# Kernel optimization log

Measured on AMD Instinct MI355X. Metric: run time of the kernel, lower is better.

The kernel has to match this reference:

```python
import jax, jax.numpy as jnp
import numpy as np

NEG_SLOPE = 0.2  # PyG GATConv LeakyReLU slope
BN_EPS = 1e-5
NUM_GRAPHS = 16


def gat_conv(x, src, dst, W, a_src, a_dst, bias, heads, out_c, concat):
    N = x.shape[0]
    h = (x @ W).reshape(N, heads, out_c)                      # [N,H,C]
    s_src = jnp.sum(h * a_src, axis=-1)                       # [N,H] per-node src score
    s_dst = jnp.sum(h * a_dst, axis=-1)                       # [N,H]
    e = jax.nn.leaky_relu(s_src[src] + s_dst[dst], NEG_SLOPE) # [E,H]
    # segment softmax over incoming edges of each dst node
    m = jax.ops.segment_max(e, dst, num_segments=N)           # [N,H]
    ex = jnp.exp(e - m[dst])
    denom = jax.ops.segment_sum(ex, dst, num_segments=N)      # [N,H]
    alpha = ex / (denom[dst] + 1e-16)                         # [E,H]
    msg = h[src] * alpha[:, :, None]                          # [E,H,C]
    out = jax.ops.segment_sum(msg, dst, num_segments=N)       # [N,H,C]
    out = out.reshape(N, heads * out_c) if concat else out.mean(axis=1)
    return out + bias


def batchnorm_eval(x, gamma, beta, rm, rv):
    return (x - rm) * jax.lax.rsqrt(rv + BN_EPS) * gamma + beta


def setup_inputs() -> dict:
    key = jax.random.key(0)
    ks = jax.random.split(key, 16)
    N, E, Fin, Hc, Hd, Emb = 20000, 640000, 128, 64, 4, 128
    x = jax.random.normal(ks[0], (N, Fin), dtype=jnp.float32)
    edge_index = jax.random.randint(ks[1], (2, E), 0, N, dtype=jnp.int64)
    batch = jnp.sort(jax.random.randint(ks[2], (N,), 0, NUM_GRAPHS, dtype=jnp.int64))
    sc1 = 1.0 / np.sqrt(Fin)
    sc2 = 1.0 / np.sqrt(Hc * Hd)
    return {
        "x": x, "edge_index": edge_index, "batch": batch,
        "W1": jax.random.normal(ks[3], (Fin, Hd * Hc), dtype=jnp.float32) * sc1,
        "a_src1": jax.random.normal(ks[4], (Hd, Hc), dtype=jnp.float32) * sc2,
        "a_dst1": jax.random.normal(ks[5], (Hd, Hc), dtype=jnp.float32) * sc2,
        "b1": jnp.zeros((Hd * Hc,), jnp.float32),
        "g1": jnp.ones((Hd * Hc,), jnp.float32),
        "be1": jnp.zeros((Hd * Hc,), jnp.float32),
        "rm1": jax.random.normal(ks[6], (Hd * Hc,), dtype=jnp.float32) * 0.1,
        "rv1": jnp.ones((Hd * Hc,), jnp.float32),
        "W2": jax.random.normal(ks[7], (Hd * Hc, Emb), dtype=jnp.float32) * sc2,
        "a_src2": jax.random.normal(ks[8], (1, Emb), dtype=jnp.float32) / np.sqrt(Emb),
        "a_dst2": jax.random.normal(ks[9], (1, Emb), dtype=jnp.float32) / np.sqrt(Emb),
        "b2": jnp.zeros((Emb,), jnp.float32),
        "g2": jnp.ones((Emb,), jnp.float32),
        "be2": jnp.zeros((Emb,), jnp.float32),
        "rm2": jax.random.normal(ks[10], (Emb,), dtype=jnp.float32) * 0.1,
        "rv2": jnp.ones((Emb,), jnp.float32),
    }


def reference(x, edge_index, batch, W1, a_src1, a_dst1, b1, g1, be1, rm1, rv1,
              W2, a_src2, a_dst2, b2, g2, be2, rm2, rv2):
    N = x.shape[0]
    loops = jnp.arange(N, dtype=edge_index.dtype)
    src = jnp.concatenate([edge_index[0], loops])  # PyG GATConv adds self-loops
    dst = jnp.concatenate([edge_index[1], loops])
    # layer 1: heads=4, concat
    h = gat_conv(x, src, dst, W1, a_src1, a_dst1, b1, heads=4, out_c=64, concat=True)
    h = batchnorm_eval(h, g1, be1, rm1, rv1)
    h = jax.nn.elu(h)  # dropout is identity in eval mode
    # layer 2: heads=1, no concat (mean over heads)
    h = gat_conv(h, src, dst, W2, a_src2, a_dst2, b2, heads=1, out_c=128, concat=False)
    h = batchnorm_eval(h, g2, be2, rm2, rv2)
    # global mean pool per graph
    sums = jax.ops.segment_sum(h, batch, num_segments=NUM_GRAPHS)
    cnts = jax.ops.segment_sum(jnp.ones((N,), h.dtype), batch, num_segments=NUM_GRAPHS)
    return sums / jnp.maximum(cnts, 1.0)[:, None]
```

## Files before the change

kernel.cpp:

```cpp
#include <hip/hip_runtime.h>
#include <hip/hip_bf16.h>
#include <math.h>

#define NEG_SLOPE 0.2f
#define BN_EPS 1e-5f
#define ELLW 128
#define SCLAMP 60.0f
#define LDP 68

typedef __attribute__((ext_vector_type(8))) short bf16x8;
typedef __attribute__((ext_vector_type(4))) float f32x4;

__device__ __forceinline__ void atomAddF(float* p, float v) { unsafeAtomicAdd(p, v); }
__device__ __forceinline__ float bf_lo(unsigned u) { return __uint_as_float(u << 16); }
__device__ __forceinline__ float bf_hi(unsigned u) { return __uint_as_float(u & 0xffff0000u); }
__device__ __forceinline__ float lk(float x) { return x > 0.f ? x : NEG_SLOPE * x; }
__device__ __forceinline__ float eexp(float x) { return __expf(fminf(x, SCLAMP)); }
__device__ __forceinline__ unsigned packbf(float lo, float hi) {
    return (unsigned)__bfloat16_as_ushort(__float2bfloat16(lo)) |
           ((unsigned)__bfloat16_as_ushort(__float2bfloat16(hi)) << 16);
}

__global__ __launch_bounds__(256) void prep_kernel(const float* __restrict__ x,
                                                   const float* __restrict__ W1,
                                                   const float* __restrict__ W2,
                                                   __hip_bfloat16* __restrict__ xbf,
                                                   __hip_bfloat16* __restrict__ WT1,
                                                   __hip_bfloat16* __restrict__ WT2,
                                                   int* __restrict__ zb, int zwords,
                                                   int n4) {
    int i = blockIdx.x * blockDim.x + threadIdx.x;
    if (i < n4) {
        float4 v = ((const float4*)x)[i];
        ushort4 st;
        st.x = __bfloat16_as_ushort(__float2bfloat16(v.x));
        st.y = __bfloat16_as_ushort(__float2bfloat16(v.y));
        st.z = __bfloat16_as_ushort(__float2bfloat16(v.z));
        st.w = __bfloat16_as_ushort(__float2bfloat16(v.w));
        *(ushort4*)(xbf + (size_t)i * 4) = st;
        return;
    }
    int j = i - n4;
    if (j < 128 * 256) {
        int k = j >> 8, n = j & 255;
        WT1[(size_t)n * 128 + k] = __float2bfloat16(W1[j]);
        return;
    }
    j -= 128 * 256;
    if (j < 256 * 128) {
        int k = j >> 7, n = j & 127;
        WT2[(size_t)n * 256 + k] = __float2bfloat16(W2[j]);
        return;
    }
    j -= 256 * 128;
    if (j < zwords) zb[j] = 0;
}

__global__ __launch_bounds__(256) void scatter_kernel(const int* __restrict__ src,
                                                      const int* __restrict__ dst,
                                                      int* __restrict__ cnt,
                                                      unsigned short* __restrict__ ell,
                                                      int N, int E, int Etot) {
    const int xcd = blockIdx.x & 7;
    const int slice = blockIdx.x >> 3;
    const int nslices = gridDim.x >> 3;
    const int d0 = (int)((long)xcd * N / 8);
    const int d1 = (int)((long)(xcd + 1) * N / 8);
    for (int e = slice * 256 + threadIdx.x; e < Etot; e += nslices * 256) {
        int d = (e < E) ? dst[e] : e - E;
        if (d < d0 || d >= d1) continue;
        int s = (e < E) ? src[e] : d;
        int pos = atomicAdd(cnt + d, 1);
        if (pos < ELLW) ell[(size_t)d * ELLW + pos] = (unsigned short)s;
    }
}

__global__ __launch_bounds__(256) void gemm_score_kernel(const __hip_bfloat16* __restrict__ A,
                                                         const __hip_bfloat16* __restrict__ BT,
                                                         __hip_bfloat16* __restrict__ C,
                                                         const float* __restrict__ asrc,
                                                         const float* __restrict__ adst,
                                                         float* __restrict__ ssrc,
                                                         float* __restrict__ sdst,
                                                         int M, int N, int K, int heads) {
    __shared__ __hip_bfloat16 As[64 * LDP];
    __shared__ __hip_bfloat16 Bs[64 * LDP];
    const int tid = threadIdx.x;
    const int w = tid >> 6;
    const int lane = tid & 63;
    const int q = lane >> 4;
    const int r16 = lane & 15;
    const int bm = blockIdx.y * 64;
    const int bn = blockIdx.x * 64;
    const int lrow = tid >> 3;
    const int lseg = tid & 7;
    f32x4 acc[4] = {};

    for (int k0 = 0; k0 < K; k0 += 64) {
#pragma unroll
        for (int half = 0; half < 2; ++half) {
            int row = lrow + half * 32;
            int ga = min(bm + row, M - 1);
            *(bf16x8*)(&As[row * LDP + lseg * 8]) =
                *(const bf16x8*)(A + (size_t)ga * K + k0 + lseg * 8);
            *(bf16x8*)(&Bs[row * LDP + lseg * 8]) =
                *(const bf16x8*)(BT + (size_t)(bn + row) * K + k0 + lseg * 8);
        }
        __syncthreads();
#pragma unroll
        for (int kk = 0; kk < 64; kk += 32) {
            bf16x8 a = *(const bf16x8*)(&As[(w * 16 + r16) * LDP + kk + q * 8]);
#pragma unroll
            for (int t = 0; t < 4; ++t) {
                bf16x8 b = *(const bf16x8*)(&Bs[(t * 16 + r16) * LDP + kk + q * 8]);
                acc[t] = __builtin_amdgcn_mfma_f32_16x16x32_bf16(a, b, acc[t], 0, 0, 0);
            }
        }
        __syncthreads();
    }
#pragma unroll
    for (int t = 0; t < 4; ++t)
#pragma unroll
        for (int r = 0; r < 4; ++r) {
            int row = bm + w * 16 + q * 4 + r;
            if (row < M)
                C[(size_t)row * N + bn + t * 16 + r16] = __float2bfloat16(acc[t][r]);
        }
    if (heads) {
        const int h = (heads == 4) ? blockIdx.x : 0;
        float asv[4], adv[4];
#pragma unroll
        for (int t = 0; t < 4; ++t) {
            int col = bn + t * 16 + r16;
            asv[t] = asrc[col]; adv[t] = adst[col];
        }
#pragma unroll
        for (int r = 0; r < 4; ++r) {
            int row = bm + w * 16 + q * 4 + r;
            float ss = 0.f, sd = 0.f;
#pragma unroll
            for (int t = 0; t < 4; ++t) { ss += acc[t][r] * asv[t]; sd += acc[t][r] * adv[t]; }
#pragma unroll
            for (int mask = 1; mask <= 8; mask <<= 1) {
                ss += __shfl_xor(ss, mask);
                sd += __shfl_xor(sd, mask);
            }
            if (r16 == 0 && row < M) {
                atomAddF(&ssrc[(size_t)row * heads + h], ss);
                atomAddF(&sdst[(size_t)row * heads + h], sd);
            }
        }
    }
}

__global__ __launch_bounds__(256) void fused1_kernel(const unsigned short* __restrict__ ell,
                                                     const int* __restrict__ cnt,
                                                     const float* __restrict__ ssrc,
                                                     const float* __restrict__ sdst,
                                                     const __hip_bfloat16* __restrict__ h1,
                                                     const float* __restrict__ b,
                                                     const float* __restrict__ g,
                                                     const float* __restrict__ be,
                                                     const float* __restrict__ rm,
                                                     const float* __restrict__ rv,
                                                     __hip_bfloat16* __restrict__ out1,
                                                     int N) {
    __shared__ float sex[4][ELLW * 4];
    __shared__ unsigned soff[4][ELLW];
    const int w = threadIdx.x >> 6;
    const int lane = threadIdx.x & 63;
    const int n = blockIdx.x * 4 + w;
    if (n >= N) return;
    const int degn = min(cnt[n], ELLW);
    const unsigned short* __restrict__ row = ell + (size_t)n * ELLW;
    const float4 sd4 = *(const float4*)(sdst + (size_t)n * 4);

    float4 d4 = {0.f, 0.f, 0.f, 0.f};
    for (int i = lane; i < degn; i += 64) {
        int s = row[i];
        float4 sc = *(const float4*)(ssrc + (size_t)s * 4);
        float4 e4;
        e4.x = eexp(lk(sc.x + sd4.x)); e4.y = eexp(lk(sc.y + sd4.y));
        e4.z = eexp(lk(sc.z + sd4.z)); e4.w = eexp(lk(sc.w + sd4.w));
        *(float4*)(&sex[w][i * 4]) = e4;
        soff[w][i] = (unsigned)s << 9;
        d4.x += e4.x; d4.y += e4.y; d4.z += e4.z; d4.w += e4.w;
    }
    if (lane == 0 && (degn & 1)) {
        float4 z = {0.f, 0.f, 0.f, 0.f};
        *(float4*)(&sex[w][degn * 4]) = z;
        soff[w][degn] = 0;
    }
#pragma unroll
    for (int o = 32; o; o >>= 1) {
        d4.x += __shfl_xor(d4.x, o); d4.y += __shfl_xor(d4.y, o);
        d4.z += __shfl_xor(d4.z, o); d4.w += __shfl_xor(d4.w, o);
    }

    const int half = lane >> 5;
    const int l32 = lane & 31;
    const int ch = l32 * 8;
    const int h = l32 >> 3;
    const unsigned choff = (unsigned)(l32 * 16);
    const float denh = h == 0 ? d4.x : h == 1 ? d4.y : h == 2 ? d4.z : d4.w;
    const float rden = 1.f / (denh + 1e-16f);
    const unsigned char* __restrict__ hb = (const unsigned char*)h1;
    const int degp = (degn + 1) & ~1;

    f32x4 a0 = {0.f, 0.f, 0.f, 0.f}, a1 = {0.f, 0.f, 0.f, 0.f};
    int i = 0;
    for (; i + 8 <= degp; i += 8) {
        unsigned off[4]; float av[4]; uint4 u[4];
#pragma unroll
        for (int k = 0; k < 4; ++k) {
            int e = i + 2 * k + half;
            off[k] = soff[w][e] + choff;
            av[k] = sex[w][e * 4 + h];
        }
#pragma unroll
        for (int k = 0; k < 4; ++k) u[k] = *(const uint4*)(hb + off[k]);
#pragma unroll
        for (int k = 0; k < 4; ++k) {
            a0.x += av[k] * bf_lo(u[k].x); a0.y += av[k] * bf_hi(u[k].x);
            a0.z += av[k] * bf_lo(u[k].y); a0.w += av[k] * bf_hi(u[k].y);
            a1.x += av[k] * bf_lo(u[k].z); a1.y += av[k] * bf_hi(u[k].z);
            a1.z += av[k] * bf_lo(u[k].w); a1.w += av[k] * bf_hi(u[k].w);
        }
    }
    for (; i < degp; i += 2) {
        int e = i + half;
        unsigned off = soff[w][e] + choff;
        float av = sex[w][e * 4 + h];
        uint4 u = *(const uint4*)(hb + off);
        a0.x += av * bf_lo(u.x); a0.y += av * bf_hi(u.x);
        a0.z += av * bf_lo(u.y); a0.w += av * bf_hi(u.y);
        a1.x += av * bf_lo(u.z); a1.y += av * bf_hi(u.z);
        a1.z += av * bf_lo(u.w); a1.w += av * bf_hi(u.w);
    }
    a0.x += __shfl_xor(a0.x, 32); a0.y += __shfl_xor(a0.y, 32);
    a0.z += __shfl_xor(a0.z, 32); a0.w += __shfl_xor(a0.w, 32);
    a1.x += __shfl_xor(a1.x, 32); a1.y += __shfl_xor(a1.y, 32);
    a1.z += __shfl_xor(a1.z, 32); a1.w += __shfl_xor(a1.w, 32);

    float4 bb0 = *(const float4*)(b + ch),  bb1 = *(const float4*)(b + ch + 4);
    float4 gg0 = *(const float4*)(g + ch),  gg1 = *(const float4*)(g + ch + 4);
    float4 ee0 = *(const float4*)(be + ch), ee1 = *(const float4*)(be + ch + 4);
    float4 mm0 = *(const float4*)(rm + ch), mm1 = *(const float4*)(rm + ch + 4);
    float4 vv0 = *(const float4*)(rv + ch), vv1 = *(const float4*)(rv + ch + 4);
    float o0 = (a0.x * rden + bb0.x - mm0.x) * rsqrtf(vv0.x + BN_EPS) * gg0.x + ee0.x;
    float o1 = (a0.y * rden + bb0.y - mm0.y) * rsqrtf(vv0.y + BN_EPS) * gg0.y + ee0.y;
    float o2 = (a0.z * rden + bb0.z - mm0.z) * rsqrtf(vv0.z + BN_EPS) * gg0.z + ee0.z;
    float o3 = (a0.w * rden + bb0.w - mm0.w) * rsqrtf(vv0.w + BN_EPS) * gg0.w + ee0.w;
    float o4 = (a1.x * rden + bb1.x - mm1.x) * rsqrtf(vv1.x + BN_EPS) * gg1.x + ee1.x;
    float o5 = (a1.y * rden + bb1.y - mm1.y) * rsqrtf(vv1.y + BN_EPS) * gg1.y + ee1.y;
    float o6 = (a1.z * rden + bb1.z - mm1.z) * rsqrtf(vv1.z + BN_EPS) * gg1.z + ee1.z;
    float o7 = (a1.w * rden + bb1.w - mm1.w) * rsqrtf(vv1.w + BN_EPS) * gg1.w + ee1.w;
    o0 = o0 > 0.f ? o0 : expm1f(o0); o1 = o1 > 0.f ? o1 : expm1f(o1);
    o2 = o2 > 0.f ? o2 : expm1f(o2); o3 = o3 > 0.f ? o3 : expm1f(o3);
    o4 = o4 > 0.f ? o4 : expm1f(o4); o5 = o5 > 0.f ? o5 : expm1f(o5);
    o6 = o6 > 0.f ? o6 : expm1f(o6); o7 = o7 > 0.f ? o7 : expm1f(o7);
    if (half == 0) {
        uint4 st;
        st.x = packbf(o0, o1); st.y = packbf(o2, o3);
        st.z = packbf(o4, o5); st.w = packbf(o6, o7);
        *(uint4*)(out1 + (size_t)n * 256 + ch) = st;
    }
}

__global__ __launch_bounds__(256) void fused2_kernel(const unsigned short* __restrict__ ell,
                                                     const int* __restrict__ cnt,
                                                     const float* __restrict__ ssrc,
                                                     const float* __restrict__ sdst,
                                                     const __hip_bfloat16* __restrict__ h2,
                                                     const float* __restrict__ b,
                                                     const float* __restrict__ g,
                                                     const float* __restrict__ be,
                                                     const float* __restrict__ rm,
                                                     const float* __restrict__ rv,
                                                     __hip_bfloat16* __restrict__ out2,
                                                     int N) {
    __shared__ float sex[4][ELLW];
    __shared__ unsigned soff[4][ELLW];
    const int w = threadIdx.x >> 6;
    const int lane = threadIdx.x & 63;
    const int n = blockIdx.x * 4 + w;
    if (n >= N) return;
    const int degn = min(cnt[n], ELLW);
    const unsigned short* __restrict__ row = ell + (size_t)n * ELLW;
    const float sd = sdst[n];

    float den = 0.f;
    for (int i = lane; i < degn; i += 64) {
        int s = row[i];
        float e = eexp(lk(ssrc[s] + sd));
        sex[w][i] = e;
        soff[w][i] = (unsigned)s << 8;
        den += e;
    }
    if (lane == 0 && (degn & 1)) { sex[w][degn] = 0.f; soff[w][degn] = 0; }
#pragma unroll
    for (int o = 32; o; o >>= 1) den += __shfl_xor(den, o);
    const float rden = 1.f / (den + 1e-16f);

    const int half = lane >> 5;
    const int l32 = lane & 31;
    const int ch = l32 * 4;
    const unsigned choff = (unsigned)(l32 * 8);
    const unsigned char* __restrict__ hb = (const unsigned char*)h2;
    const int degp = (degn + 1) & ~1;

    f32x4 acc = {0.f, 0.f, 0.f, 0.f};
    int i = 0;
    for (; i + 8 <= degp; i += 8) {
        unsigned off[4]; float av[4]; uint2 u[4];
#pragma unroll
        for (int k = 0; k < 4; ++k) {
            int e = i + 2 * k + half;
            off[k] = soff[w][e] + choff;
            av[k] = sex[w][e];
        }
#pragma unroll
        for (int k = 0; k < 4; ++k) u[k] = *(const uint2*)(hb + off[k]);
#pragma unroll
        for (int k = 0; k < 4; ++k) {
            acc.x += av[k] * bf_lo(u[k].x); acc.y += av[k] * bf_hi(u[k].x);
            acc.z += av[k] * bf_lo(u[k].y); acc.w += av[k] * bf_hi(u[k].y);
        }
    }
    for (; i < degp; i += 2) {
        int e = i + half;
        unsigned off = soff[w][e] + choff;
        float av = sex[w][e];
        uint2 u = *(const uint2*)(hb + off);
        acc.x += av * bf_lo(u.x); acc.y += av * bf_hi(u.x);
        acc.z += av * bf_lo(u.y); acc.w += av * bf_hi(u.y);
    }
    acc.x += __shfl_xor(acc.x, 32); acc.y += __shfl_xor(acc.y, 32);
    acc.z += __shfl_xor(acc.z, 32); acc.w += __shfl_xor(acc.w, 32);

    if (half == 0) {
        float4 bb = *(const float4*)(b + ch), gg = *(const float4*)(g + ch);
        float4 ee = *(const float4*)(be + ch), mm = *(const float4*)(rm + ch);
        float4 vv = *(const float4*)(rv + ch);
        float o0 = (acc.x * rden + bb.x - mm.x) * rsqrtf(vv.x + BN_EPS) * gg.x + ee.x;
        float o1 = (acc.y * rden + bb.y - mm.y) * rsqrtf(vv.y + BN_EPS) * gg.y + ee.y;
        float o2 = (acc.z * rden + bb.z - mm.z) * rsqrtf(vv.z + BN_EPS) * gg.z + ee.z;
        float o3 = (acc.w * rden + bb.w - mm.w) * rsqrtf(vv.w + BN_EPS) * gg.w + ee.w;
        ushort2 s01, s23;
        s01.x = __bfloat16_as_ushort(__float2bfloat16(o0));
        s01.y = __bfloat16_as_ushort(__float2bfloat16(o1));
        s23.x = __bfloat16_as_ushort(__float2bfloat16(o2));
        s23.y = __bfloat16_as_ushort(__float2bfloat16(o3));
        uint2 st = { *(unsigned*)&s01, *(unsigned*)&s23 };
        *(uint2*)(out2 + (size_t)n * 128 + ch) = st;
    }
}

__global__ __launch_bounds__(128) void pool_kernel(const __hip_bfloat16* __restrict__ out2,
                                                   const int* __restrict__ batch,
                                                   float* __restrict__ pool,
                                                   int N, int npb) {
    const int j = threadIdx.x;
    int n0 = blockIdx.x * npb;
    int n1 = min(n0 + npb, N);
    if (n0 >= n1) return;
    int curg = batch[n0];
    float acc = 0.f;
    for (int n = n0; n < n1; ++n) {
        int gr = batch[n];
        if (gr != curg) {
            atomAddF(pool + (size_t)curg * 128 + j, acc);
            acc = 0.f; curg = gr;
        }
        acc += __bfloat162float(out2[(size_t)n * 128 + j]);
    }
    atomAddF(pool + (size_t)curg * 128 + j, acc);
}

__device__ __forceinline__ int lowerBound(const int* __restrict__ a, int n, int v) {
    int lo = 0, hi = n;
    while (lo < hi) {
        int mid = (lo + hi) >> 1;
        if (a[mid] < v) lo = mid + 1; else hi = mid;
    }
    return lo;
}

__global__ __launch_bounds__(256) void final_kernel(const float* __restrict__ pool,
                                                    const int* __restrict__ batch,
                                                    float* __restrict__ out, int N) {
    int i = blockIdx.x * blockDim.x + threadIdx.x;
    int g = i >> 7;
    int c = lowerBound(batch, N, g + 1) - lowerBound(batch, N, g);
    out[i] = pool[i] / fmaxf((float)c, 1.f);
}

extern "C" void kernel_launch(void* const* d_in, const int* in_sizes, int n_in,
                              void* d_out, int out_size, void* d_ws, size_t ws_size,
                              hipStream_t stream) {
    const float* x    = (const float*)d_in[0];
    const int* ei     = (const int*)d_in[1];
    const int* batch  = (const int*)d_in[2];
    const float* W1   = (const float*)d_in[3];
    const float* as1  = (const float*)d_in[4];
    const float* ad1  = (const float*)d_in[5];
    const float* b1   = (const float*)d_in[6];
    const float* g1   = (const float*)d_in[7];
    const float* be1  = (const float*)d_in[8];
    const float* rm1  = (const float*)d_in[9];
    const float* rv1  = (const float*)d_in[10];
    const float* W2   = (const float*)d_in[11];
    const float* as2  = (const float*)d_in[12];
    const float* ad2  = (const float*)d_in[13];
    const float* b2   = (const float*)d_in[14];
    const float* g2   = (const float*)d_in[15];
    const float* be2  = (const float*)d_in[16];
    const float* rm2  = (const float*)d_in[17];
    const float* rv2  = (const float*)d_in[18];
    float* out = (float*)d_out;

    const int N = in_sizes[0] / 128;
    const int E = in_sizes[1] / 2;
    const int Etot = E + N;
    const int* src = ei;
    const int* dst = ei + E;

    char* p = (char*)d_ws;
    auto alloc = [&](size_t bytes) { char* r = p; p += (bytes + 255) & ~(size_t)255; return r; };
    __hip_bfloat16* h1   = (__hip_bfloat16*)alloc((size_t)N * 256 * 2);
    __hip_bfloat16* out1 = (__hip_bfloat16*)alloc((size_t)N * 256 * 2);
    __hip_bfloat16* out2 = (__hip_bfloat16*)alloc((size_t)N * 128 * 2);
    __hip_bfloat16* xbf  = (__hip_bfloat16*)alloc((size_t)N * 128 * 2);
    __hip_bfloat16* WT1  = (__hip_bfloat16*)alloc(256 * 128 * 2);
    __hip_bfloat16* WT2  = (__hip_bfloat16*)alloc(128 * 256 * 2);
    const int zwords     = N * 10 + 2048 + N;
    char* zbase          = alloc((size_t)zwords * 4);
    float* ssrc1         = (float*)zbase;
    float* sdst1         = ssrc1 + (size_t)N * 4;
    float* ssrc2         = sdst1 + (size_t)N * 4;
    float* sdst2         = ssrc2 + N;
    float* pool          = sdst2 + N;
    int*   cnt           = (int*)(pool + 2048);
    unsigned short* ell  = (unsigned short*)alloc((size_t)N * ELLW * 2);
    __hip_bfloat16* h2   = h1;

    const int n4 = N * 128 / 4;
    const int ptot = n4 + 2 * 128 * 256 + zwords;
    prep_kernel<<<(ptot + 255) / 256, 256, 0, stream>>>(x, W1, W2, xbf, WT1, WT2,
                                                        (int*)zbase, zwords, n4);
    scatter_kernel<<<2048, 256, 0, stream>>>(src, dst, cnt, ell, N, E, Etot);

    gemm_score_kernel<<<dim3(256 / 64, (N + 63) / 64), 256, 0, stream>>>(
        xbf, WT1, h1, as1, ad1, ssrc1, sdst1, N, 256, 128, 4);
    fused1_kernel<<<(N + 3) / 4, 256, 0, stream>>>(ell, cnt, ssrc1, sdst1, h1,
                                                   b1, g1, be1, rm1, rv1, out1, N);
    gemm_score_kernel<<<dim3(128 / 64, (N + 63) / 64), 256, 0, stream>>>(
        out1, WT2, h2, as2, ad2, ssrc2, sdst2, N, 128, 256, 1);
    fused2_kernel<<<(N + 3) / 4, 256, 0, stream>>>(ell, cnt, ssrc2, sdst2, h2,
                                                   b2, g2, be2, rm2, rv2, out2, N);

    pool_kernel<<<(N + 19) / 20, 128, 0, stream>>>(out2, batch, pool, N, 20);
    final_kernel<<<8, 256, 0, stream>>>(pool, batch, out, N);
}
```

Baseline: 234.6 us.

## Merge edge scatter with layer-1 GEMM in one launch; deepen gather unroll

The edge-to-ELL scatter and the first GEMM+score kernel are independent, so they are merged into one launch. The first nbg blocks do GEMM tiles and the remaining 2048 do scatter, letting both run concurrently and saving one launch. The aggregation loops in both fused kernels now unroll 8 gathers per iteration instead of 4 to keep more memory loads in flight. In exchange, scatter blocks carry the GEMM's shared-memory footprint, and the deeper unroll raises register pressure. The XCD partitioning for scatter now comes from gb&7 rather than a dense block index, which still maps consistently.

```diff
diff --git a/kernel.cpp b/kernel.cpp
--- a/kernel.cpp
+++ b/kernel.cpp
@@ -56,14 +56,107 @@
     if (j < zwords) zb[j] = 0;
 }
 
-__global__ __launch_bounds__(256) void scatter_kernel(const int* __restrict__ src,
-                                                      const int* __restrict__ dst,
-                                                      int* __restrict__ cnt,
-                                                      unsigned short* __restrict__ ell,
-                                                      int N, int E, int Etot) {
-    const int xcd = blockIdx.x & 7;
-    const int slice = blockIdx.x >> 3;
-    const int nslices = gridDim.x >> 3;
+__device__ __forceinline__ void gemm_body(const __hip_bfloat16* __restrict__ A,
+                                          const __hip_bfloat16* __restrict__ BT,
+                                          __hip_bfloat16* __restrict__ C,
+                                          const float* __restrict__ asrc,
+                                          const float* __restrict__ adst,
+                                          float* __restrict__ ssrc,
+                                          float* __restrict__ sdst,
+                                          int M, int N, int K, int heads,
+                                          int bx, int by) {
+    __shared__ __hip_bfloat16 As[64 * LDP];
+    __shared__ __hip_bfloat16 Bs[64 * LDP];
+    const int tid = threadIdx.x;
+    const int w = tid >> 6;
+    const int lane = tid & 63;
+    const int q = lane >> 4;
+    const int r16 = lane & 15;
+    const int bm = by * 64;
+    const int bn = bx * 64;
+    const int lrow = tid >> 3;
+    const int lseg = tid & 7;
+    f32x4 acc[4] = {};
+
+    for (int k0 = 0; k0 < K; k0 += 64) {
+#pragma unroll
+        for (int half = 0; half < 2; ++half) {
+            int row = lrow + half * 32;
+            int ga = min(bm + row, M - 1);
+            *(bf16x8*)(&As[row * LDP + lseg * 8]) =
+                *(const bf16x8*)(A + (size_t)ga * K + k0 + lseg * 8);
+            *(bf16x8*)(&Bs[row * LDP + lseg * 8]) =
+                *(const bf16x8*)(BT + (size_t)(bn + row) * K + k0 + lseg * 8);
+        }
+        __syncthreads();
+#pragma unroll
+        for (int kk = 0; kk < 64; kk += 32) {
+            bf16x8 a = *(const bf16x8*)(&As[(w * 16 + r16) * LDP + kk + q * 8]);
+#pragma unroll
+            for (int t = 0; t < 4; ++t) {
+                bf16x8 b = *(const bf16x8*)(&Bs[(t * 16 + r16) * LDP + kk + q * 8]);
+                acc[t] = __builtin_amdgcn_mfma_f32_16x16x32_bf16(a, b, acc[t], 0, 0, 0);
+            }
+        }
+        __syncthreads();
+    }
+#pragma unroll
+    for (int t = 0; t < 4; ++t)
+#pragma unroll
+        for (int r = 0; r < 4; ++r) {
+            int row = bm + w * 16 + q * 4 + r;
+            if (row < M)
+                C[(size_t)row * N + bn + t * 16 + r16] = __float2bfloat16(acc[t][r]);
+        }
+    if (heads) {
+        const int h = (heads == 4) ? bx : 0;
+        float asv[4], adv[4];
+#pragma unroll
+        for (int t = 0; t < 4; ++t) {
+            int col = bn + t * 16 + r16;
+            asv[t] = asrc[col]; adv[t] = adst[col];
+        }
+#pragma unroll
+        for (int r = 0; r < 4; ++r) {
+            int row = bm + w * 16 + q * 4 + r;
+            float ss = 0.f, sd = 0.f;
+#pragma unroll
+            for (int t = 0; t < 4; ++t) { ss += acc[t][r] * asv[t]; sd += acc[t][r] * adv[t]; }
+#pragma unroll
+            for (int mask = 1; mask <= 8; mask <<= 1) {
+                ss += __shfl_xor(ss, mask);
+                sd += __shfl_xor(sd, mask);
+            }
+            if (r16 == 0 && row < M) {
+                atomAddF(&ssrc[(size_t)row * heads + h], ss);
+                atomAddF(&sdst[(size_t)row * heads + h], sd);
+            }
+        }
+    }
+}
+
+__global__ __launch_bounds__(256) void sg1_kernel(const __hip_bfloat16* __restrict__ A,
+                                                  const __hip_bfloat16* __restrict__ BT,
+                                                  __hip_bfloat16* __restrict__ C,
+                                                  const float* __restrict__ asrc,
+                                                  const float* __restrict__ adst,
+                                                  float* __restrict__ ssrc,
+                                                  float* __restrict__ sdst,
+                                                  int M, int nbg,
+                                                  const int* __restrict__ src,
+                                                  const int* __restrict__ dst,
+                                                  int* __restrict__ cnt,
+                                                  unsigned short* __restrict__ ell,
+                                                  int N, int E, int Etot) {
+    const int gb = blockIdx.x;
+    if (gb < nbg) {
+        gemm_body(A, BT, C, asrc, adst, ssrc, sdst, M, 256, 128, 4, gb & 3, gb >> 2);
+        return;
+    }
+    const int xcd = gb & 7;
+    const int sb = gb - nbg;
+    const int slice = sb >> 3;
+    const int nslices = (gridDim.x - nbg) >> 3;
     const int d0 = (int)((long)xcd * N / 8);
     const int d1 = (int)((long)(xcd + 1) * N / 8);
     for (int e = slice * 256 + threadIdx.x; e < Etot; e += nslices * 256) {
@@ -83,74 +176,7 @@
                                                          float* __restrict__ ssrc,
                                                          float* __restrict__ sdst,
                                                          int M, int N, int K, int heads) {
-    __shared__ __hip_bfloat16 As[64 * LDP];
-    __shared__ __hip_bfloat16 Bs[64 * LDP];
-    const int tid = threadIdx.x;
-    const int w = tid >> 6;
-    const int lane = tid & 63;
-    const int q = lane >> 4;
-    const int r16 = lane & 15;
-    const int bm = blockIdx.y * 64;
-    const int bn = blockIdx.x * 64;
-    const int lrow = tid >> 3;
-    const int lseg = tid & 7;
-    f32x4 acc[4] = {};
-
-    for (int k0 = 0; k0 < K; k0 += 64) {
-#pragma unroll
-        for (int half = 0; half < 2; ++half) {
-            int row = lrow + half * 32;
-            int ga = min(bm + row, M - 1);
-            *(bf16x8*)(&As[row * LDP + lseg * 8]) =
-                *(const bf16x8*)(A + (size_t)ga * K + k0 + lseg * 8);
-            *(bf16x8*)(&Bs[row * LDP + lseg * 8]) =
-                *(const bf16x8*)(BT + (size_t)(bn + row) * K + k0 + lseg * 8);
-        }
-        __syncthreads();
-#pragma unroll
-        for (int kk = 0; kk < 64; kk += 32) {
-            bf16x8 a = *(const bf16x8*)(&As[(w * 16 + r16) * LDP + kk + q * 8]);
-#pragma unroll
-            for (int t = 0; t < 4; ++t) {
-                bf16x8 b = *(const bf16x8*)(&Bs[(t * 16 + r16) * LDP + kk + q * 8]);
-                acc[t] = __builtin_amdgcn_mfma_f32_16x16x32_bf16(a, b, acc[t], 0, 0, 0);
-            }
-        }
-        __syncthreads();
-    }
-#pragma unroll
-    for (int t = 0; t < 4; ++t)
-#pragma unroll
-        for (int r = 0; r < 4; ++r) {
-            int row = bm + w * 16 + q * 4 + r;
-            if (row < M)
-                C[(size_t)row * N + bn + t * 16 + r16] = __float2bfloat16(acc[t][r]);
-        }
-    if (heads) {
-        const int h = (heads == 4) ? blockIdx.x : 0;
-        float asv[4], adv[4];
-#pragma unroll
-        for (int t = 0; t < 4; ++t) {
-            int col = bn + t * 16 + r16;
-            asv[t] = asrc[col]; adv[t] = adst[col];
-        }
-#pragma unroll
-        for (int r = 0; r < 4; ++r) {
-            int row = bm + w * 16 + q * 4 + r;
-            float ss = 0.f, sd = 0.f;
-#pragma unroll
-            for (int t = 0; t < 4; ++t) { ss += acc[t][r] * asv[t]; sd += acc[t][r] * adv[t]; }
-#pragma unroll
-            for (int mask = 1; mask <= 8; mask <<= 1) {
-                ss += __shfl_xor(ss, mask);
-                sd += __shfl_xor(sd, mask);
-            }
-            if (r16 == 0 && row < M) {
-                atomAddF(&ssrc[(size_t)row * heads + h], ss);
-                atomAddF(&sdst[(size_t)row * heads + h], sd);
-            }
-        }
-    }
+    gemm_body(A, BT, C, asrc, adst, ssrc, sdst, M, N, K, heads, blockIdx.x, blockIdx.y);
 }
 
 __global__ __launch_bounds__(256) void fused1_kernel(const unsigned short* __restrict__ ell,
@@ -209,18 +235,18 @@
 
     f32x4 a0 = {0.f, 0.f, 0.f, 0.f}, a1 = {0.f, 0.f, 0.f, 0.f};
     int i = 0;
-    for (; i + 8 <= degp; i += 8) {
-        unsigned off[4]; float av[4]; uint4 u[4];
-#pragma unroll
-        for (int k = 0; k < 4; ++k) {
+    for (; i + 16 <= degp; i += 16) {
+        unsigned off[8]; float av[8]; uint4 u[8];
+#pragma unroll
+        for (int k = 0; k < 8; ++k) {
             int e = i + 2 * k + half;
             off[k] = soff[w][e] + choff;
             av[k] = sex[w][e * 4 + h];
         }
 #pragma unroll
-        for (int k = 0; k < 4; ++k) u[k] = *(const uint4*)(hb + off[k]);
-#pragma unroll
-        for (int k = 0; k < 4; ++k) {
+        for (int k = 0; k < 8; ++k) u[k] = *(const uint4*)(hb + off[k]);
+#pragma unroll
+        for (int k = 0; k < 8; ++k) {
             a0.x += av[k] * bf_lo(u[k].x); a0.y += av[k] * bf_hi(u[k].x);
             a0.z += av[k] * bf_lo(u[k].y); a0.w += av[k] * bf_hi(u[k].y);
             a1.x += av[k] * bf_lo(u[k].z); a1.y += av[k] * bf_hi(u[k].z);
@@ -311,18 +337,18 @@
 
     f32x4 acc = {0.f, 0.f, 0.f, 0.f};
     int i = 0;
-    for (; i + 8 <= degp; i += 8) {
-        unsigned off[4]; float av[4]; uint2 u[4];
-#pragma unroll
-        for (int k = 0; k < 4; ++k) {
+    for (; i + 16 <= degp; i += 16) {
+        unsigned off[8]; float av[8]; uint2 u[8];
+#pragma unroll
+        for (int k = 0; k < 8; ++k) {
             int e = i + 2 * k + half;
             off[k] = soff[w][e] + choff;
             av[k] = sex[w][e];
         }
 #pragma unroll
-        for (int k = 0; k < 4; ++k) u[k] = *(const uint2*)(hb + off[k]);
-#pragma unroll
-        for (int k = 0; k < 4; ++k) {
+        for (int k = 0; k < 8; ++k) u[k] = *(const uint2*)(hb + off[k]);
+#pragma unroll
+        for (int k = 0; k < 8; ++k) {
             acc.x += av[k] * bf_lo(u[k].x); acc.y += av[k] * bf_hi(u[k].x);
             acc.z += av[k] * bf_lo(u[k].y); acc.w += av[k] * bf_hi(u[k].y);
         }
@@ -448,10 +474,11 @@
     const int ptot = n4 + 2 * 128 * 256 + zwords;
     prep_kernel<<<(ptot + 255) / 256, 256, 0, stream>>>(x, W1, W2, xbf, WT1, WT2,
                                                         (int*)zbase, zwords, n4);
-    scatter_kernel<<<2048, 256, 0, stream>>>(src, dst, cnt, ell, N, E, Etot);
-
-    gemm_score_kernel<<<dim3(256 / 64, (N + 63) / 64), 256, 0, stream>>>(
-        xbf, WT1, h1, as1, ad1, ssrc1, sdst1, N, 256, 128, 4);
+
+    const int nbg1 = 4 * ((N + 63) / 64);
+    sg1_kernel<<<nbg1 + 2048, 256, 0, stream>>>(xbf, WT1, h1, as1, ad1, ssrc1, sdst1,
+                                                N, nbg1, src, dst, cnt, ell, N, E, Etot);
+
     fused1_kernel<<<(N + 3) / 4, 256, 0, stream>>>(ell, cnt, ssrc1, sdst1, h1,
                                                    b1, g1, be1, rm1, rv1, out1, N);
     gemm_score_kernel<<<dim3(128 / 64, (N + 63) / 64), 256, 0, stream>>>(
```

Measured after the change: 233.8 us. Within noise of the previous version (-0.3%).
